# Optimization experiments

Hardware: AMD Instinct MI355X
Metric: run time of the kernel (lower is better)

Reference implementation:

```python
import jax, jax.numpy as jnp
import numpy as np

TOP_K = 2  # num_experts_per_tok


def setup_inputs() -> dict:
    key = jax.random.key(0)
    k1, k2, k3, k4 = jax.random.split(key, 4)
    T, H, I, E = 1024, 2048, 768, 8  # tokens, hidden, moe_intermediate, num_experts
    return {
        "hidden_states": jax.random.normal(k1, (T, H), jnp.float32),
        "gate_w": jax.random.normal(k2, (E, H), jnp.float32) * 0.02,      # router nn.Linear(H,E) weight
        "w_gate_up": jax.random.normal(k3, (E, 2 * I, H), jnp.float32) * 0.02,  # merged gate+up proj per expert
        "w_down": jax.random.normal(k4, (E, H, I), jnp.float32) * 0.02,   # down proj per expert
    }


def _moe(hidden_states, gate_w, w_gate_up, w_down):
    T, H = hidden_states.shape
    E = gate_w.shape[0]
    # router: softmax in fp32, then top-k, renormalize (matches _forward_local)
    logits = hidden_states @ gate_w.T                         # [T, E]
    probs = jax.nn.softmax(logits.astype(jnp.float32), axis=-1)
    top_w, top_i = jax.lax.top_k(probs, TOP_K)                # [T, K]
    top_w = top_w / jnp.sum(top_w, axis=-1, keepdims=True)
    top_w = top_w.astype(hidden_states.dtype)
    # per-token combine weight for each expert (top-k indices are unique per token)
    comb = jnp.zeros((T, E), hidden_states.dtype).at[
        jnp.arange(T)[:, None], top_i
    ].add(top_w)                                              # [T, E]

    def body(acc, xs):
        wgu, wd, cw = xs            # [2I,H], [H,I], [T]
        gu = hidden_states @ wgu.T  # [T, 2I]
        g, u = jnp.split(gu, 2, axis=-1)
        h = jax.nn.silu(g) * u      # SiluAndMul
        out = h @ wd.T              # [T, H]
        return acc + out * cw[:, None], None

    init = jnp.zeros_like(hidden_states)
    out, _ = jax.lax.scan(body, init, (w_gate_up, w_down, comb.T))
    return out


def reference(hidden_states, gate_w, w_gate_up, w_down):
    return _moe(hidden_states, gate_w, w_gate_up, w_down)
```

## Files before the change

### kernel.cpp

```cpp
#include <hip/hip_runtime.h>
#include <hip/hip_bf16.h>

typedef unsigned short u16;
typedef __bf16 bf16x8 __attribute__((ext_vector_type(8)));
typedef float f32x4 __attribute__((ext_vector_type(4)));

#define T_TOK 1024
#define HID   2048
#define IMM   768
#define NE    8
#define TWOI  1536

static __device__ __forceinline__ u16 f2bf(float f) {
  unsigned u = __float_as_uint(f);
  u += 0x7FFFu + ((u >> 16) & 1u);
  return (u16)(u >> 16);
}
static __device__ __forceinline__ float bf2f(u16 s) {
  return __uint_as_float(((unsigned)s) << 16);
}

__global__ __launch_bounds__(64) void router_kernel(
    const float* __restrict__ hid, const float* __restrict__ gw,
    int* __restrict__ cnt, int* __restrict__ tok_of, float* __restrict__ wslot)
{
  const int t = blockIdx.x;
  const int lane = threadIdx.x;
  float acc[NE];
#pragma unroll
  for (int e = 0; e < NE; ++e) acc[e] = 0.f;
  const float4* h4 = (const float4*)(hid + (long)t * HID);
#pragma unroll 2
  for (int c = lane; c < HID / 4; c += 64) {
    float4 x = h4[c];
#pragma unroll
    for (int e = 0; e < NE; ++e) {
      float4 w = ((const float4*)(gw + e * HID))[c];
      acc[e] += x.x * w.x + x.y * w.y + x.z * w.z + x.w * w.w;
    }
  }
#pragma unroll
  for (int e = 0; e < NE; ++e) {
    float v = acc[e];
#pragma unroll
    for (int off = 32; off > 0; off >>= 1) v += __shfl_xor(v, off, 64);
    acc[e] = v;
  }
  if (lane == 0) {
    float mx = acc[0];
#pragma unroll
    for (int e = 1; e < NE; ++e) mx = fmaxf(mx, acc[e]);
    float p[NE]; float s = 0.f;
#pragma unroll
    for (int e = 0; e < NE; ++e) { p[e] = expf(acc[e] - mx); s += p[e]; }
    const float inv = 1.f / s;
    float p1 = -1.f, p2 = -1.f; int i1 = 0, i2 = 0;
#pragma unroll
    for (int e = 0; e < NE; ++e) {
      float pe = p[e] * inv;
      if (pe > p1)      { p2 = p1; i2 = i1; p1 = pe; i1 = e; }
      else if (pe > p2) { p2 = pe; i2 = e; }
    }
    const float wsum = p1 + p2;
    int s1 = atomicAdd(&cnt[i1], 1);
    tok_of[i1 * T_TOK + s1] = t;
    wslot[i1 * T_TOK + s1] = p1 / wsum;
    int s2 = atomicAdd(&cnt[i2], 1);
    tok_of[i2 * T_TOK + s2] = t;
    wslot[i2 * T_TOK + s2] = p2 / wsum;
  }
}

__global__ __launch_bounds__(256) void cvt_kernel(
    const float* __restrict__ in, u16* __restrict__ out)
{
  const int i = blockIdx.x * 256 + threadIdx.x;
  float4 x = ((const float4*)in)[i];
  ushort4 o;
  o.x = f2bf(x.x); o.y = f2bf(x.y); o.z = f2bf(x.z); o.w = f2bf(x.w);
  ((ushort4*)out)[i] = o;
}

template<int K, bool GATHER_A, bool OUT_ATOMIC>
__global__ __launch_bounds__(256, 2) void gemm_moe(
    const u16* __restrict__ A, int lda, long a_zoff,
    const float* __restrict__ B, long b_zoff,
    const int* __restrict__ tok_of, const int* __restrict__ cnt,
    u16* __restrict__ Cb, float* __restrict__ Cf, int ldc, long c_zoff)
{
  constexpr int BM = 128, BN = 128, BK = 32;
  constexpr int LSTR = BK + 8;
  constexpr int NKT = K / BK;
  static_assert(NKT >= 2 && (K % BK) == 0, "K must be multiple of 32, >=64");

  const int z = blockIdx.z;
  const int nrow = cnt[z];
  const long m0 = (long)blockIdx.x * BM;
  if (m0 >= nrow) return;

  __shared__ __align__(16) u16 As[2][BM * LSTR];
  __shared__ __align__(16) u16 Bs[2][BN * LSTR];

  const int tid  = threadIdx.x;
  const int lane = tid & 63;
  const int wave = tid >> 6;
  const int wm = wave >> 1, wn = wave & 1;
  const int lrow = lane & 15;
  const int lk   = (lane >> 4) << 3;

  const long n0 = (long)blockIdx.y * BN;
  const float* Bb = B + b_zoff * z + n0 * (long)K;

  const int r0  = tid >> 2;
  const int cs0 = (tid & 3) << 3;

  const u16 *ap0, *ap1;
  if constexpr (GATHER_A) {
    ap0 = A + (long)tok_of[z * T_TOK + m0 + r0] * lda + cs0;
    ap1 = A + (long)tok_of[z * T_TOK + m0 + r0 + 64] * lda + cs0;
  } else {
    ap0 = A + a_zoff * z + (m0 + r0) * (long)lda + cs0;
    ap1 = ap0 + 64l * lda;
  }

  uint4 sa0, sa1; float4 sb0a, sb0b, sb1a, sb1b;

  auto gload = [&](int kk) {
    sa0 = *(const uint4*)(ap0 + kk);
    sa1 = *(const uint4*)(ap1 + kk);
    const float* bp = Bb + (long)r0 * K + kk + cs0;
    sb0a = *(const float4*)bp;
    sb0b = *(const float4*)(bp + 4);
    sb1a = *(const float4*)(bp + 64l * K);
    sb1b = *(const float4*)(bp + 64l * K + 4);
  };
  auto packb = [&](const float4& f0, const float4& f1) -> uint4 {
    return make_uint4(
      (unsigned)f2bf(f0.x) | ((unsigned)f2bf(f0.y) << 16),
      (unsigned)f2bf(f0.z) | ((unsigned)f2bf(f0.w) << 16),
      (unsigned)f2bf(f1.x) | ((unsigned)f2bf(f1.y) << 16),
      (unsigned)f2bf(f1.z) | ((unsigned)f2bf(f1.w) << 16));
  };
  auto swrite = [&](int buf) {
    *(uint4*)&As[buf][r0 * LSTR + cs0]        = sa0;
    *(uint4*)&As[buf][(r0 + 64) * LSTR + cs0] = sa1;
    *(uint4*)&Bs[buf][r0 * LSTR + cs0]        = packb(sb0a, sb0b);
    *(uint4*)&Bs[buf][(r0 + 64) * LSTR + cs0] = packb(sb1a, sb1b);
  };

  f32x4 acc[4][4];
  const f32x4 zero4 = {0.f, 0.f, 0.f, 0.f};
#pragma unroll
  for (int m = 0; m < 4; ++m)
#pragma unroll
    for (int n = 0; n < 4; ++n) acc[m][n] = zero4;

  auto compute = [&](int buf) {
    bf16x8 af[4], bfr[4];
#pragma unroll
    for (int m = 0; m < 4; ++m)
      af[m] = *(const bf16x8*)&As[buf][(wm * 64 + m * 16 + lrow) * LSTR + lk];
#pragma unroll
    for (int n = 0; n < 4; ++n)
      bfr[n] = *(const bf16x8*)&Bs[buf][(wn * 64 + n * 16 + lrow) * LSTR + lk];
#pragma unroll
    for (int m = 0; m < 4; ++m)
#pragma unroll
      for (int n = 0; n < 4; ++n)
        acc[m][n] = __builtin_amdgcn_mfma_f32_16x16x32_bf16(af[m], bfr[n], acc[m][n], 0, 0, 0);
  };

  gload(0);
  swrite(0);
  __syncthreads();
  int cur = 0;
#pragma unroll 1
  for (int kt = 0; kt < NKT - 1; ++kt) {
    gload((kt + 1) * BK);
    compute(cur);
    swrite(cur ^ 1);
    __syncthreads();
    cur ^= 1;
  }
  compute(cur);

  const int rloc = wm * 64 + ((lane >> 4) << 2);
  const long cbase = n0 + wn * 64 + lrow;
#pragma unroll
  for (int m = 0; m < 4; ++m) {
#pragma unroll
    for (int n = 0; n < 4; ++n) {
#pragma unroll
      for (int j = 0; j < 4; ++j) {
        const long slot = m0 + rloc + m * 16 + j;
        const long col = cbase + n * 16;
        if constexpr (OUT_ATOMIC) {
          if (slot < nrow) {
            const long tok = tok_of[z * T_TOK + slot];
            atomicAdd(Cf + tok * ldc + col, acc[m][n][j]);
          }
        } else {
          Cb[c_zoff * z + slot * ldc + col] = f2bf(acc[m][n][j]);
        }
      }
    }
  }
}

__global__ __launch_bounds__(256) void silu_kernel(
    const u16* __restrict__ gu, const float* __restrict__ wslot,
    u16* __restrict__ hp)
{
  const int c = blockIdx.x * 256 + threadIdx.x;
  const int idx = c << 3;
  const int g = idx / IMM;
  const int i0 = idx - g * IMM;
  const u16* gp = gu + (long)g * TWOI + i0;
  uint4 gv = *(const uint4*)gp;
  uint4 uv = *(const uint4*)(gp + IMM);
  const float cw = wslot[g];
  const unsigned* gwv = (const unsigned*)&gv;
  const unsigned* uwv = (const unsigned*)&uv;
  unsigned outw[4];
#pragma unroll
  for (int q = 0; q < 4; ++q) {
    float g0 = bf2f((u16)(gwv[q] & 0xFFFFu));
    float g1 = bf2f((u16)(gwv[q] >> 16));
    float u0 = bf2f((u16)(uwv[q] & 0xFFFFu));
    float u1 = bf2f((u16)(uwv[q] >> 16));
    float h0 = cw * u0 * (g0 / (1.f + __expf(-g0)));
    float h1 = cw * u1 * (g1 / (1.f + __expf(-g1)));
    outw[q] = (unsigned)f2bf(h0) | ((unsigned)f2bf(h1) << 16);
  }
  *(uint4*)(hp + (long)g * IMM + i0) = make_uint4(outw[0], outw[1], outw[2], outw[3]);
}

extern "C" void kernel_launch(void* const* d_in, const int* in_sizes, int n_in,
                              void* d_out, int out_size, void* d_ws, size_t ws_size,
                              hipStream_t stream) {
  const float* hid = (const float*)d_in[0];
  const float* gw  = (const float*)d_in[1];
  const float* wgu = (const float*)d_in[2];
  const float* wd  = (const float*)d_in[3];
  float* out = (float*)d_out;

  char* ws = (char*)d_ws;
  u16*   hidb   = (u16*)ws;
  int*   cnt    = (int*)(ws + (4l << 20));
  int*   tok_of = (int*)(ws + (4l << 20) + (1l << 12));
  float* wslot  = (float*)(ws + (4l << 20) + (1l << 12) + (1l << 15));
  u16*   gu     = (u16*)(ws + (4l << 20) + (1l << 17));
  u16*   hp     = (u16*)(ws + (4l << 20) + (1l << 17)
                            + (long)NE * T_TOK * TWOI * 2);

  hipMemsetAsync(d_out, 0, (size_t)out_size * sizeof(float), stream);
  hipMemsetAsync(ws + (4l << 20), 0, (1l << 17), stream);

  router_kernel<<<T_TOK, 64, 0, stream>>>(hid, gw, cnt, tok_of, wslot);
  cvt_kernel<<<(T_TOK * HID / 4) / 256, 256, 0, stream>>>(hid, hidb);
  gemm_moe<HID, true, false><<<dim3(T_TOK / 128, TWOI / 128, NE), 256, 0, stream>>>(
      hidb, HID, 0, wgu, (long)TWOI * HID,
      tok_of, cnt, gu, nullptr, TWOI, (long)T_TOK * TWOI);
  silu_kernel<<<(NE * T_TOK * IMM / 8) / 256, 256, 0, stream>>>(gu, wslot, hp);
  gemm_moe<IMM, false, true><<<dim3(T_TOK / 128, HID / 128, NE), 256, 0, stream>>>(
      hp, IMM, (long)T_TOK * IMM, wd, (long)HID * IMM,
      tok_of, cnt, nullptr, out, HID, 0);
}
```

Before: 386.6 us.

## Shrink MoE GEMM tiles to 64x64 and remap blocks across XCDs

Each MoE GEMM tile drops from 128x128 to 64x64, with a 2x2 MFMA accumulator per wave and a higher occupancy hint. A 1D grid is decoded so that all blocks sharing an N column range of one expert's weights land on the same XCD. The aim is finer granularity for ragged per-expert token counts, fewer wasted tiles, and better L2 reuse of the fp32 weights. The k-loop is unrolled by two with explicit register double-buffering. Smaller tiles mean each weight tile is reloaded and converted to bf16 by twice as many M-blocks, and the down projection issues more atomics.

```diff
diff --git a/kernel.cpp b/kernel.cpp
--- a/kernel.cpp
+++ b/kernel.cpp
@@ -81,21 +81,28 @@
   ((ushort4*)out)[i] = o;
 }
 
-template<int K, bool GATHER_A, bool OUT_ATOMIC>
-__global__ __launch_bounds__(256, 2) void gemm_moe(
+template<int K, int NT, bool GATHER_A, bool OUT_ATOMIC>
+__global__ __launch_bounds__(256, 4) void gemm_moe(
     const u16* __restrict__ A, int lda, long a_zoff,
     const float* __restrict__ B, long b_zoff,
     const int* __restrict__ tok_of, const int* __restrict__ cnt,
     u16* __restrict__ Cb, float* __restrict__ Cf, int ldc, long c_zoff)
 {
-  constexpr int BM = 128, BN = 128, BK = 32;
+  constexpr int BM = 64, BN = 64, BK = 32;
   constexpr int LSTR = BK + 8;
   constexpr int NKT = K / BK;
-  static_assert(NKT >= 2 && (K % BK) == 0, "K must be multiple of 32, >=64");
-
-  const int z = blockIdx.z;
-  const int nrow = cnt[z];
-  const long m0 = (long)blockIdx.x * BM;
+  static_assert(NKT >= 4 && (NKT % 2) == 0, "K must be multiple of 64, >=128");
+
+  const int id  = blockIdx.x;
+  const int xcd = id & 7;
+  const int p   = id >> 3;
+  const int mi  = p & 15;
+  const int q   = p >> 4;
+  const int e   = q & 7;
+  const int n_t = (q >> 3) + (NT / 8) * xcd;
+
+  const int nrow = cnt[e];
+  const int m0 = mi * BM;
   if (m0 >= nrow) return;
 
   __shared__ __align__(16) u16 As[2][BM * LSTR];
@@ -108,31 +115,25 @@
   const int lrow = lane & 15;
   const int lk   = (lane >> 4) << 3;
 
-  const long n0 = (long)blockIdx.y * BN;
-  const float* Bb = B + b_zoff * z + n0 * (long)K;
+  const long n0 = (long)n_t * BN;
 
   const int r0  = tid >> 2;
   const int cs0 = (tid & 3) << 3;
 
-  const u16 *ap0, *ap1;
+  const u16* ap;
   if constexpr (GATHER_A) {
-    ap0 = A + (long)tok_of[z * T_TOK + m0 + r0] * lda + cs0;
-    ap1 = A + (long)tok_of[z * T_TOK + m0 + r0 + 64] * lda + cs0;
+    ap = A + (long)tok_of[e * T_TOK + m0 + r0] * lda + cs0;
   } else {
-    ap0 = A + a_zoff * z + (m0 + r0) * (long)lda + cs0;
-    ap1 = ap0 + 64l * lda;
-  }
-
-  uint4 sa0, sa1; float4 sb0a, sb0b, sb1a, sb1b;
-
-  auto gload = [&](int kk) {
-    sa0 = *(const uint4*)(ap0 + kk);
-    sa1 = *(const uint4*)(ap1 + kk);
-    const float* bp = Bb + (long)r0 * K + kk + cs0;
-    sb0a = *(const float4*)bp;
-    sb0b = *(const float4*)(bp + 4);
-    sb1a = *(const float4*)(bp + 64l * K);
-    sb1b = *(const float4*)(bp + 64l * K + 4);
+    ap = A + a_zoff * e + (m0 + r0) * (long)lda + cs0;
+  }
+  const float* bp = B + b_zoff * e + (n0 + r0) * (long)K + cs0;
+
+  uint4 ra_a, rb_a; float4 ra_b0, ra_b1, rb_b0, rb_b1;
+
+  auto gload = [&](uint4& sa, float4& sb0, float4& sb1, int kk) {
+    sa  = *(const uint4*)(ap + kk);
+    sb0 = *(const float4*)(bp + kk);
+    sb1 = *(const float4*)(bp + kk + 4);
   };
   auto packb = [&](const float4& f0, const float4& f1) -> uint4 {
     return make_uint4(
@@ -141,66 +142,71 @@
       (unsigned)f2bf(f1.x) | ((unsigned)f2bf(f1.y) << 16),
       (unsigned)f2bf(f1.z) | ((unsigned)f2bf(f1.w) << 16));
   };
-  auto swrite = [&](int buf) {
-    *(uint4*)&As[buf][r0 * LSTR + cs0]        = sa0;
-    *(uint4*)&As[buf][(r0 + 64) * LSTR + cs0] = sa1;
-    *(uint4*)&Bs[buf][r0 * LSTR + cs0]        = packb(sb0a, sb0b);
-    *(uint4*)&Bs[buf][(r0 + 64) * LSTR + cs0] = packb(sb1a, sb1b);
-  };
-
-  f32x4 acc[4][4];
+  auto swrite = [&](int buf, const uint4& sa, const float4& sb0, const float4& sb1) {
+    *(uint4*)&As[buf][r0 * LSTR + cs0] = sa;
+    *(uint4*)&Bs[buf][r0 * LSTR + cs0] = packb(sb0, sb1);
+  };
+
+  f32x4 acc[2][2];
   const f32x4 zero4 = {0.f, 0.f, 0.f, 0.f};
 #pragma unroll
-  for (int m = 0; m < 4; ++m)
-#pragma unroll
-    for (int n = 0; n < 4; ++n) acc[m][n] = zero4;
+  for (int m = 0; m < 2; ++m)
+#pragma unroll
+    for (int n = 0; n < 2; ++n) acc[m][n] = zero4;
 
   auto compute = [&](int buf) {
-    bf16x8 af[4], bfr[4];
-#pragma unroll
-    for (int m = 0; m < 4; ++m)
-      af[m] = *(const bf16x8*)&As[buf][(wm * 64 + m * 16 + lrow) * LSTR + lk];
-#pragma unroll
-    for (int n = 0; n < 4; ++n)
-      bfr[n] = *(const bf16x8*)&Bs[buf][(wn * 64 + n * 16 + lrow) * LSTR + lk];
-#pragma unroll
-    for (int m = 0; m < 4; ++m)
-#pragma unroll
-      for (int n = 0; n < 4; ++n)
-        acc[m][n] = __builtin_amdgcn_mfma_f32_16x16x32_bf16(af[m], bfr[n], acc[m][n], 0, 0, 0);
-  };
-
-  gload(0);
-  swrite(0);
+    bf16x8 af[2], bfv[2];
+#pragma unroll
+    for (int m = 0; m < 2; ++m)
+      af[m] = *(const bf16x8*)&As[buf][(wm * 32 + m * 16 + lrow) * LSTR + lk];
+#pragma unroll
+    for (int n = 0; n < 2; ++n)
+      bfv[n] = *(const bf16x8*)&Bs[buf][(wn * 32 + n * 16 + lrow) * LSTR + lk];
+#pragma unroll
+    for (int m = 0; m < 2; ++m)
+#pragma unroll
+      for (int n = 0; n < 2; ++n)
+        acc[m][n] = __builtin_amdgcn_mfma_f32_16x16x32_bf16(af[m], bfv[n], acc[m][n], 0, 0, 0);
+  };
+
+  gload(ra_a, ra_b0, ra_b1, 0);
+  gload(rb_a, rb_b0, rb_b1, BK);
+  swrite(0, ra_a, ra_b0, ra_b1);
   __syncthreads();
-  int cur = 0;
+
 #pragma unroll 1
-  for (int kt = 0; kt < NKT - 1; ++kt) {
-    gload((kt + 1) * BK);
-    compute(cur);
-    swrite(cur ^ 1);
+  for (int kt = 0; kt < NKT - 2; kt += 2) {
+    gload(ra_a, ra_b0, ra_b1, (kt + 2) * BK);
+    compute(0);
+    swrite(1, rb_a, rb_b0, rb_b1);
     __syncthreads();
-    cur ^= 1;
-  }
-  compute(cur);
-
-  const int rloc = wm * 64 + ((lane >> 4) << 2);
-  const long cbase = n0 + wn * 64 + lrow;
-#pragma unroll
-  for (int m = 0; m < 4; ++m) {
-#pragma unroll
-    for (int n = 0; n < 4; ++n) {
+    gload(rb_a, rb_b0, rb_b1, (kt + 3) * BK);
+    compute(1);
+    swrite(0, ra_a, ra_b0, ra_b1);
+    __syncthreads();
+  }
+  compute(0);
+  swrite(1, rb_a, rb_b0, rb_b1);
+  __syncthreads();
+  compute(1);
+
+  const int rloc = wm * 32 + ((lane >> 4) << 2);
+  const long cbase = n0 + wn * 32 + lrow;
+#pragma unroll
+  for (int m = 0; m < 2; ++m) {
+#pragma unroll
+    for (int n = 0; n < 2; ++n) {
 #pragma unroll
       for (int j = 0; j < 4; ++j) {
         const long slot = m0 + rloc + m * 16 + j;
         const long col = cbase + n * 16;
         if constexpr (OUT_ATOMIC) {
           if (slot < nrow) {
-            const long tok = tok_of[z * T_TOK + slot];
+            const long tok = tok_of[e * T_TOK + slot];
             atomicAdd(Cf + tok * ldc + col, acc[m][n][j]);
           }
         } else {
-          Cb[c_zoff * z + slot * ldc + col] = f2bf(acc[m][n][j]);
+          Cb[c_zoff * e + slot * ldc + col] = f2bf(acc[m][n][j]);
         }
       }
     }
@@ -258,11 +264,11 @@
 
   router_kernel<<<T_TOK, 64, 0, stream>>>(hid, gw, cnt, tok_of, wslot);
   cvt_kernel<<<(T_TOK * HID / 4) / 256, 256, 0, stream>>>(hid, hidb);
-  gemm_moe<HID, true, false><<<dim3(T_TOK / 128, TWOI / 128, NE), 256, 0, stream>>>(
+  gemm_moe<HID, TWOI / 64, true, false><<<128 * (TWOI / 64), 256, 0, stream>>>(
       hidb, HID, 0, wgu, (long)TWOI * HID,
       tok_of, cnt, gu, nullptr, TWOI, (long)T_TOK * TWOI);
   silu_kernel<<<(NE * T_TOK * IMM / 8) / 256, 256, 0, stream>>>(gu, wslot, hp);
-  gemm_moe<IMM, false, true><<<dim3(T_TOK / 128, HID / 128, NE), 256, 0, stream>>>(
+  gemm_moe<IMM, HID / 64, false, true><<<128 * (HID / 64), 256, 0, stream>>>(
       hp, IMM, (long)T_TOK * IMM, wd, (long)HID * IMM,
       tok_of, cnt, nullptr, out, HID, 0);
 }
```

After: 394.2 us. About the same (+2.0%).

## Split-K both MoE GEMMs in two, reducing partials in SiLU or via atomics

Applied to the files above, without the earlier changes.

Both expert GEMMs now split the K dimension into two halves launched as extra grid-z slices, which doubles the number of workgroups so the sparse per-expert grid (many early-exit blocks) fills the GPU better. The gate/up partial sums are written to two bf16 buffers and summed inside the SiLU kernel. The down projection already accumulates through fp32 atomics, so its halves add straight into the output. Launch bounds also move to 4 waves per EU. The cost is extra partial-buffer traffic, double the atomics on the output, and bf16 rounding of each partial before summation.

```diff
diff --git a/kernel.cpp b/kernel.cpp
--- a/kernel.cpp
+++ b/kernel.cpp
@@ -81,20 +81,26 @@
   ((ushort4*)out)[i] = o;
 }
 
-template<int K, bool GATHER_A, bool OUT_ATOMIC>
-__global__ __launch_bounds__(256, 2) void gemm_moe(
+template<int K, int KS, bool GATHER_A, bool OUT_ATOMIC>
+__global__ __launch_bounds__(256, 4) void gemm_moe(
     const u16* __restrict__ A, int lda, long a_zoff,
     const float* __restrict__ B, long b_zoff,
     const int* __restrict__ tok_of, const int* __restrict__ cnt,
-    u16* __restrict__ Cb, float* __restrict__ Cf, int ldc, long c_zoff)
+    u16* __restrict__ Cb, long ks_coff, float* __restrict__ Cf,
+    int ldc, long c_zoff)
 {
   constexpr int BM = 128, BN = 128, BK = 32;
   constexpr int LSTR = BK + 8;
-  constexpr int NKT = K / BK;
-  static_assert(NKT >= 2 && (K % BK) == 0, "K must be multiple of 32, >=64");
-
-  const int z = blockIdx.z;
-  const int nrow = cnt[z];
+  constexpr int KH  = K / KS;
+  constexpr int NKT = KH / BK;
+  static_assert(NKT >= 2 && (KH % BK) == 0, "K chunk must be multiple of 32, >=64");
+
+  const int z  = blockIdx.z;
+  const int e  = z & (NE - 1);
+  const int ks = z >> 3;
+  const int kb = ks * KH;
+
+  const int nrow = cnt[e];
   const long m0 = (long)blockIdx.x * BM;
   if (m0 >= nrow) return;
 
@@ -109,17 +115,17 @@
   const int lk   = (lane >> 4) << 3;
 
   const long n0 = (long)blockIdx.y * BN;
-  const float* Bb = B + b_zoff * z + n0 * (long)K;
+  const float* Bb = B + b_zoff * e + n0 * (long)K;
 
   const int r0  = tid >> 2;
   const int cs0 = (tid & 3) << 3;
 
   const u16 *ap0, *ap1;
   if constexpr (GATHER_A) {
-    ap0 = A + (long)tok_of[z * T_TOK + m0 + r0] * lda + cs0;
-    ap1 = A + (long)tok_of[z * T_TOK + m0 + r0 + 64] * lda + cs0;
+    ap0 = A + (long)tok_of[e * T_TOK + m0 + r0] * lda + kb + cs0;
+    ap1 = A + (long)tok_of[e * T_TOK + m0 + r0 + 64] * lda + kb + cs0;
   } else {
-    ap0 = A + a_zoff * z + (m0 + r0) * (long)lda + cs0;
+    ap0 = A + a_zoff * e + (m0 + r0) * (long)lda + kb + cs0;
     ap1 = ap0 + 64l * lda;
   }
 
@@ -128,7 +134,7 @@
   auto gload = [&](int kk) {
     sa0 = *(const uint4*)(ap0 + kk);
     sa1 = *(const uint4*)(ap1 + kk);
-    const float* bp = Bb + (long)r0 * K + kk + cs0;
+    const float* bp = Bb + (long)r0 * K + kb + kk + cs0;
     sb0a = *(const float4*)bp;
     sb0b = *(const float4*)(bp + 4);
     sb1a = *(const float4*)(bp + 64l * K);
@@ -186,6 +192,7 @@
 
   const int rloc = wm * 64 + ((lane >> 4) << 2);
   const long cbase = n0 + wn * 64 + lrow;
+  u16* CbE = Cb + c_zoff * e + (long)ks * ks_coff;
 #pragma unroll
   for (int m = 0; m < 4; ++m) {
 #pragma unroll
@@ -196,11 +203,11 @@
         const long col = cbase + n * 16;
         if constexpr (OUT_ATOMIC) {
           if (slot < nrow) {
-            const long tok = tok_of[z * T_TOK + slot];
+            const long tok = tok_of[e * T_TOK + slot];
             atomicAdd(Cf + tok * ldc + col, acc[m][n][j]);
           }
         } else {
-          Cb[c_zoff * z + slot * ldc + col] = f2bf(acc[m][n][j]);
+          CbE[slot * ldc + col] = f2bf(acc[m][n][j]);
         }
       }
     }
@@ -208,28 +215,33 @@
 }
 
 __global__ __launch_bounds__(256) void silu_kernel(
-    const u16* __restrict__ gu, const float* __restrict__ wslot,
+    const u16* __restrict__ gu, long part_stride, const float* __restrict__ wslot,
     u16* __restrict__ hp)
 {
   const int c = blockIdx.x * 256 + threadIdx.x;
   const int idx = c << 3;
   const int g = idx / IMM;
   const int i0 = idx - g * IMM;
-  const u16* gp = gu + (long)g * TWOI + i0;
-  uint4 gv = *(const uint4*)gp;
-  uint4 uv = *(const uint4*)(gp + IMM);
+  const u16* gp0 = gu + (long)g * TWOI + i0;
+  const u16* gp1 = gp0 + part_stride;
+  uint4 gv0 = *(const uint4*)gp0;
+  uint4 uv0 = *(const uint4*)(gp0 + IMM);
+  uint4 gv1 = *(const uint4*)gp1;
+  uint4 uv1 = *(const uint4*)(gp1 + IMM);
   const float cw = wslot[g];
-  const unsigned* gwv = (const unsigned*)&gv;
-  const unsigned* uwv = (const unsigned*)&uv;
+  const unsigned* g0w = (const unsigned*)&gv0;
+  const unsigned* u0w = (const unsigned*)&uv0;
+  const unsigned* g1w = (const unsigned*)&gv1;
+  const unsigned* u1w = (const unsigned*)&uv1;
   unsigned outw[4];
 #pragma unroll
   for (int q = 0; q < 4; ++q) {
-    float g0 = bf2f((u16)(gwv[q] & 0xFFFFu));
-    float g1 = bf2f((u16)(gwv[q] >> 16));
-    float u0 = bf2f((u16)(uwv[q] & 0xFFFFu));
-    float u1 = bf2f((u16)(uwv[q] >> 16));
-    float h0 = cw * u0 * (g0 / (1.f + __expf(-g0)));
-    float h1 = cw * u1 * (g1 / (1.f + __expf(-g1)));
+    float ga = bf2f((u16)(g0w[q] & 0xFFFFu)) + bf2f((u16)(g1w[q] & 0xFFFFu));
+    float gb = bf2f((u16)(g0w[q] >> 16))     + bf2f((u16)(g1w[q] >> 16));
+    float ua = bf2f((u16)(u0w[q] & 0xFFFFu)) + bf2f((u16)(u1w[q] & 0xFFFFu));
+    float ub = bf2f((u16)(u0w[q] >> 16))     + bf2f((u16)(u1w[q] >> 16));
+    float h0 = cw * ua * (ga / (1.f + __expf(-ga)));
+    float h1 = cw * ub * (gb / (1.f + __expf(-gb)));
     outw[q] = (unsigned)f2bf(h0) | ((unsigned)f2bf(h1) << 16);
   }
   *(uint4*)(hp + (long)g * IMM + i0) = make_uint4(outw[0], outw[1], outw[2], outw[3]);
@@ -250,19 +262,21 @@
   int*   tok_of = (int*)(ws + (4l << 20) + (1l << 12));
   float* wslot  = (float*)(ws + (4l << 20) + (1l << 12) + (1l << 15));
   u16*   gu     = (u16*)(ws + (4l << 20) + (1l << 17));
-  u16*   hp     = (u16*)(ws + (4l << 20) + (1l << 17)
-                            + (long)NE * T_TOK * TWOI * 2);
+  const long GU_PART = (long)NE * T_TOK * TWOI;
+  u16*   hp     = (u16*)(ws + (4l << 20) + (1l << 17) + 2 * GU_PART * 2);
 
   hipMemsetAsync(d_out, 0, (size_t)out_size * sizeof(float), stream);
   hipMemsetAsync(ws + (4l << 20), 0, (1l << 17), stream);
 
   router_kernel<<<T_TOK, 64, 0, stream>>>(hid, gw, cnt, tok_of, wslot);
   cvt_kernel<<<(T_TOK * HID / 4) / 256, 256, 0, stream>>>(hid, hidb);
-  gemm_moe<HID, true, false><<<dim3(T_TOK / 128, TWOI / 128, NE), 256, 0, stream>>>(
+  gemm_moe<HID, 2, true, false>
+      <<<dim3(T_TOK / 128, TWOI / 128, NE * 2), 256, 0, stream>>>(
       hidb, HID, 0, wgu, (long)TWOI * HID,
-      tok_of, cnt, gu, nullptr, TWOI, (long)T_TOK * TWOI);
-  silu_kernel<<<(NE * T_TOK * IMM / 8) / 256, 256, 0, stream>>>(gu, wslot, hp);
-  gemm_moe<IMM, false, true><<<dim3(T_TOK / 128, HID / 128, NE), 256, 0, stream>>>(
+      tok_of, cnt, gu, GU_PART, nullptr, TWOI, (long)T_TOK * TWOI);
+  silu_kernel<<<(NE * T_TOK * IMM / 8) / 256, 256, 0, stream>>>(gu, GU_PART, wslot, hp);
+  gemm_moe<IMM, 2, false, true>
+      <<<dim3(T_TOK / 128, HID / 128, NE * 2), 256, 0, stream>>>(
       hp, IMM, (long)T_TOK * IMM, wd, (long)HID * IMM,
-      tok_of, cnt, nullptr, out, HID, 0);
-}
+      tok_of, cnt, nullptr, 0, out, HID, 0);
+}
```

After: 432.3 us. +11.8%, slower.
